# Optimization experiments

Hardware: AMD Instinct MI355X
Metric: run time of the kernel (lower is better)

Reference implementation:

```python
import jax, jax.numpy as jnp
import numpy as np

N = 50000      # nodes
E = 800000     # edges (before self-loops)
IN = 128       # in_channels
HID = 64       # hidden_channels
HEADS = 2
OUT = 128      # out_channels
NEG_SLOPE = 0.2


def setup_inputs() -> dict:
    key = jax.random.key(0)
    ks = jax.random.split(key, 12)
    p = lambda k, shape: jax.random.normal(k, shape, dtype=jnp.float32) * 0.05
    return {
        "x": jax.random.normal(ks[0], (N, IN), dtype=jnp.float32),
        "edge_index": jax.random.randint(ks[1], (2, E), 0, N, dtype=jnp.int32),
        "W1": p(ks[2], (IN, HEADS * HID)),
        "a_src1": p(ks[3], (HEADS, HID)),
        "a_dst1": p(ks[4], (HEADS, HID)),
        "b1": jnp.zeros((HEADS * HID,), dtype=jnp.float32),
        "W2": p(ks[5], (HEADS * HID, OUT)),
        "a_src2": p(ks[6], (1, OUT)),
        "a_dst2": p(ks[7], (1, OUT)),
        "b2": jnp.zeros((OUT,), dtype=jnp.float32),
    }


def _gat_conv(x, src, dst, W, a_src, a_dst, b, heads, out_c, concat):
    n = x.shape[0]
    h = (x @ W).reshape(n, heads, out_c)                # [N,H,C]
    al_s = jnp.sum(h * a_src, axis=-1)                  # [N,H]
    al_d = jnp.sum(h * a_dst, axis=-1)                  # [N,H]
    e = jax.nn.leaky_relu(al_s[src] + al_d[dst], NEG_SLOPE)  # [E',H]
    # softmax over edges grouped by destination node (numerically stable)
    e_max = jax.ops.segment_max(e, dst, num_segments=n)
    ee = jnp.exp(e - e_max[dst])
    denom = jax.ops.segment_sum(ee, dst, num_segments=n)
    alpha = ee / (denom[dst] + 1e-16)                   # [E',H]
    out = jax.ops.segment_sum(alpha[:, :, None] * h[src], dst, num_segments=n)  # [N,H,C]
    out = out.reshape(n, heads * out_c) if concat else out.mean(axis=1)
    return out + b


def reference(x, edge_index, W1, a_src1, a_dst1, b1, W2, a_src2, a_dst2, b2):
    n = x.shape[0]
    loops = jnp.arange(n, dtype=edge_index.dtype)       # PyG GATConv adds self-loops
    src = jnp.concatenate([edge_index[0], loops])
    dst = jnp.concatenate([edge_index[1], loops])
    h = jax.nn.elu(_gat_conv(x, src, dst, W1, a_src1, a_dst1, b1, HEADS, HID, True))
    return _gat_conv(h, src, dst, W2, a_src2, a_dst2, b2, 1, OUT, False)
```

## Files before the change

### kernel.cpp

```cpp
#include <hip/hip_runtime.h>
#include <hip/hip_bf16.h>
#include <math.h>

#define N_NODES 50000
#define NPAD 50048
#define N_EDGES 800000
#define NEG_SLOPE 0.2f
#define NBUCK ((N_NODES + 255) / 256)
#define CCHUNK 4096
#define DCAP 8192

__device__ inline float lrelu(float x) { return fmaxf(x, NEG_SLOPE * x); }

__device__ inline unsigned bf16rne(float f) {
    unsigned u = __float_as_uint(f);
    return (u + 0x7fffu + ((u >> 16) & 1u)) >> 16;
}
__device__ inline float bf2f(unsigned h) { return __uint_as_float(h << 16); }

__global__ void zerobuf_kernel(int* __restrict__ p) {
    int i = threadIdx.x;
    if (i < NBUCK) p[i] = 0;
}

__global__ __launch_bounds__(256) void bucketcount_kernel(const int* __restrict__ ei,
                                                          int* __restrict__ gbcnt) {
    __shared__ int lc[NBUCK];
    for (int i = threadIdx.x; i < NBUCK; i += 256) lc[i] = 0;
    __syncthreads();
    int stride = gridDim.x * 256;
    for (int e = blockIdx.x * 256 + threadIdx.x; e < N_EDGES; e += stride)
        atomicAdd(&lc[ei[N_EDGES + e] >> 8], 1);
    __syncthreads();
    for (int i = threadIdx.x; i < NBUCK; i += 256)
        if (lc[i]) atomicAdd(&gbcnt[i], lc[i]);
}

__global__ __launch_bounds__(256) void scan_convw_kernel(const int* __restrict__ gbcnt,
                                                         int* __restrict__ bbase,
                                                         int* __restrict__ bcur,
                                                         const float* __restrict__ W1,
                                                         unsigned short* __restrict__ w1h,
                                                         unsigned short* __restrict__ w1l,
                                                         const float* __restrict__ W2,
                                                         unsigned short* __restrict__ w2h,
                                                         unsigned short* __restrict__ w2l) {
    int b = blockIdx.x;
    int t = threadIdx.x;
    if (b == 0) {
        __shared__ int ss[256];
        int v = (t < NBUCK) ? gbcnt[t] : 0;
        ss[t] = v;
        __syncthreads();
        for (int d = 1; d < 256; d <<= 1) {
            int u = (t >= d) ? ss[t - d] : 0;
            __syncthreads();
            ss[t] += u;
            __syncthreads();
        }
        int excl = ss[t] - v;
        if (t < NBUCK) { bbase[t] = excl; bcur[t] = excl; }
        if (t == 0) bbase[NBUCK] = N_EDGES;
    } else {
        int idx = (b - 1) * 256 + t;
        const float* W = W1;
        unsigned short* th = w1h;
        unsigned short* tl = w1l;
        if (idx >= 128 * 128) { W = W2; th = w2h; tl = w2l; idx -= 128 * 128; }
        int c = idx >> 7, k = idx & 127;
        float v = W[(size_t)k * 128 + c];
        unsigned h = bf16rne(v);
        th[idx] = (unsigned short)h;
        tl[idx] = (unsigned short)bf16rne(v - bf2f(h));
    }
}

__global__ __launch_bounds__(256) void bucketscatter_kernel(const int* __restrict__ ei,
                                                            int* __restrict__ bcur,
                                                            unsigned* __restrict__ bpairs) {
    __shared__ int cnt[NBUCK], startl[NBUCK], baseg[NBUCK], cur2[NBUCK];
    __shared__ int ss[256];
    __shared__ unsigned stage[CCHUNK];
    int t = threadIdx.x;
    int e0 = blockIdx.x * CCHUNK;
    int nume = min(CCHUNK, N_EDGES - e0);
    for (int i = t; i < NBUCK; i += 256) { cnt[i] = 0; cur2[i] = 0; }
    __syncthreads();
    int src[CCHUNK / 256], dst[CCHUNK / 256];
    #pragma unroll
    for (int j = 0; j < CCHUNK / 256; ++j) {
        int idx = t + j * 256;
        if (idx < nume) {
            src[j] = ei[e0 + idx];
            dst[j] = ei[N_EDGES + e0 + idx];
            atomicAdd(&cnt[dst[j] >> 8], 1);
        } else dst[j] = -1;
    }
    __syncthreads();
    {
        int v = (t < NBUCK) ? cnt[t] : 0;
        ss[t] = v;
        __syncthreads();
        for (int d = 1; d < 256; d <<= 1) {
            int u = (t >= d) ? ss[t - d] : 0;
            __syncthreads();
            ss[t] += u;
            __syncthreads();
        }
        if (t < NBUCK) startl[t] = ss[t] - v;
    }
    __syncthreads();
    if (t < NBUCK && cnt[t] > 0) baseg[t] = atomicAdd(&bcur[t], cnt[t]);
    __syncthreads();
    #pragma unroll
    for (int j = 0; j < CCHUNK / 256; ++j) {
        if (dst[j] >= 0) {
            int b = dst[j] >> 8;
            int slot = startl[b] + atomicAdd(&cur2[b], 1);
            stage[slot] = (unsigned)src[j] | ((unsigned)dst[j] << 16);
        }
    }
    __syncthreads();
    for (int i = t; i < nume; i += 256) {
        unsigned pk = stage[i];
        int b = pk >> 24;
        bpairs[baseg[b] + (i - startl[b])] = pk;
    }
}

__global__ __launch_bounds__(256) void csrfinalize_kernel(const unsigned* __restrict__ bpairs,
                                                          const int* __restrict__ bbase,
                                                          int* __restrict__ ptr,
                                                          unsigned short* __restrict__ csr) {
    __shared__ int cnt[256], excl[256], cur[256];
    __shared__ int ss[256];
    __shared__ unsigned P[DCAP];
    int b = blockIdx.x, t = threadIdx.x;
    int bb = bbase[b], be = bbase[b + 1];
    int n = be - bb;
    int d0 = b << 8;
    int dmax = min(256, N_NODES - d0);
    bool fits = (n <= DCAP);
    cnt[t] = 0; cur[t] = 0;
    __syncthreads();
    for (int i = t; i < n; i += 256) {
        unsigned pk = bpairs[bb + i];
        if (fits) P[i] = pk;
        atomicAdd(&cnt[(pk >> 16) & 255], 1);
    }
    __syncthreads();
    {
        int v = cnt[t];
        ss[t] = v;
        __syncthreads();
        for (int d = 1; d < 256; d <<= 1) {
            int u = (t >= d) ? ss[t - d] : 0;
            __syncthreads();
            ss[t] += u;
            __syncthreads();
        }
        excl[t] = ss[t] - v;
    }
    __syncthreads();
    if (t < dmax) ptr[d0 + t] = bb + excl[t];
    if (b == NBUCK - 1 && t == 0) ptr[N_NODES] = N_EDGES;
    for (int i = t; i < n; i += 256) {
        unsigned pk = fits ? P[i] : bpairs[bb + i];
        int ld = (pk >> 16) & 255;
        int pos = bb + excl[ld] + atomicAdd(&cur[ld], 1);
        csr[pos] = (unsigned short)(pk & 0xFFFFu);
    }
}

template <int H, int AF32>
__global__ __launch_bounds__(256) void gemm_mfma_kernel(const unsigned short* __restrict__ Ah,
                                                        const unsigned short* __restrict__ Al,
                                                        const float* __restrict__ Af,
                                                        const unsigned short* __restrict__ Bh,
                                                        const unsigned short* __restrict__ Bl,
                                                        const float* __restrict__ asrc,
                                                        const float* __restrict__ adst,
                                                        unsigned short* __restrict__ Hb,
                                                        float* __restrict__ als,
                                                        float* __restrict__ ald,
                                                        int nrows) {
    using bf16x8 = __attribute__((ext_vector_type(8))) short;
    using f32x4  = __attribute__((ext_vector_type(4))) float;
    const int lane = threadIdx.x & 63;
    const int wv = threadIdx.x >> 6;
    const int l15 = lane & 15;
    const int g = lane >> 4;
    const int lk = g * 8;
    const int rowbase = blockIdx.x * 128 + wv * 32;
    const int r0c = min(rowbase + l15, nrows - 1);
    const int r1c = min(rowbase + 16 + l15, nrows - 1);

    f32x4 acc[2][8];
    #pragma unroll
    for (int rt = 0; rt < 2; ++rt)
        #pragma unroll
        for (int ct = 0; ct < 8; ++ct) acc[rt][ct] = (f32x4){0.f, 0.f, 0.f, 0.f};

    #pragma unroll
    for (int kc = 0; kc < 4; ++kc) {
        const int ko = kc * 32 + lk;
        bf16x8 ah0, ah1, al0, al1;
        if constexpr (AF32) {
            const float* b0 = Af + (size_t)r0c * 128 + ko;
            const float* b1 = Af + (size_t)r1c * 128 + ko;
            float4 u0 = *(const float4*)b0, u1 = *(const float4*)(b0 + 4);
            float4 v0 = *(const float4*)b1, v1 = *(const float4*)(b1 + 4);
            float a0[8] = {u0.x, u0.y, u0.z, u0.w, u1.x, u1.y, u1.z, u1.w};
            float a1[8] = {v0.x, v0.y, v0.z, v0.w, v1.x, v1.y, v1.z, v1.w};
            #pragma unroll
            for (int i = 0; i < 8; ++i) {
                unsigned h0 = bf16rne(a0[i]);
                ah0[i] = (short)h0; al0[i] = (short)bf16rne(a0[i] - bf2f(h0));
                unsigned h1 = bf16rne(a1[i]);
                ah1[i] = (short)h1; al1[i] = (short)bf16rne(a1[i] - bf2f(h1));
            }
        } else {
            ah0 = *(const bf16x8*)(Ah + (size_t)(rowbase + l15) * 128 + ko);
            ah1 = *(const bf16x8*)(Ah + (size_t)(rowbase + 16 + l15) * 128 + ko);
            al0 = *(const bf16x8*)(Al + (size_t)(rowbase + l15) * 128 + ko);
            al1 = *(const bf16x8*)(Al + (size_t)(rowbase + 16 + l15) * 128 + ko);
        }
        #pragma unroll
        for (int ct = 0; ct < 8; ++ct) {
            bf16x8 bh = *(const bf16x8*)(Bh + (size_t)(ct * 16 + l15) * 128 + ko);
            bf16x8 bl = *(const bf16x8*)(Bl + (size_t)(ct * 16 + l15) * 128 + ko);
            acc[0][ct] = __builtin_amdgcn_mfma_f32_16x16x32_bf16(ah0, bh, acc[0][ct], 0, 0, 0);
            acc[0][ct] = __builtin_amdgcn_mfma_f32_16x16x32_bf16(ah0, bl, acc[0][ct], 0, 0, 0);
            acc[0][ct] = __builtin_amdgcn_mfma_f32_16x16x32_bf16(al0, bh, acc[0][ct], 0, 0, 0);
            acc[1][ct] = __builtin_amdgcn_mfma_f32_16x16x32_bf16(ah1, bh, acc[1][ct], 0, 0, 0);
            acc[1][ct] = __builtin_amdgcn_mfma_f32_16x16x32_bf16(ah1, bl, acc[1][ct], 0, 0, 0);
            acc[1][ct] = __builtin_amdgcn_mfma_f32_16x16x32_bf16(al1, bh, acc[1][ct], 0, 0, 0);
        }
    }

    float as8[8], ad8[8];
    #pragma unroll
    for (int ct = 0; ct < 8; ++ct) { as8[ct] = asrc[ct * 16 + l15]; ad8[ct] = adst[ct * 16 + l15]; }

    #pragma unroll
    for (int rt = 0; rt < 2; ++rt) {
        #pragma unroll
        for (int ct = 0; ct < 8; ++ct) {
            #pragma unroll
            for (int j = 0; j < 4; ++j) {
                int row = rowbase + rt * 16 + g * 4 + j;
                if (row < nrows)
                    Hb[(size_t)row * 128 + ct * 16 + l15] = (unsigned short)bf16rne(acc[rt][ct][j]);
            }
        }
        #pragma unroll
        for (int j = 0; j < 4; ++j) {
            int row = rowbase + rt * 16 + g * 4 + j;
            if (H == 2) {
                float sp0 = 0.f, sp1 = 0.f, dp0 = 0.f, dp1 = 0.f;
                #pragma unroll
                for (int ct = 0; ct < 4; ++ct) { sp0 += acc[rt][ct][j] * as8[ct]; dp0 += acc[rt][ct][j] * ad8[ct]; }
                #pragma unroll
                for (int ct = 4; ct < 8; ++ct) { sp1 += acc[rt][ct][j] * as8[ct]; dp1 += acc[rt][ct][j] * ad8[ct]; }
                #pragma unroll
                for (int off = 1; off < 16; off <<= 1) {
                    sp0 += __shfl_xor(sp0, off); sp1 += __shfl_xor(sp1, off);
                    dp0 += __shfl_xor(dp0, off); dp1 += __shfl_xor(dp1, off);
                }
                if (l15 == 0 && row < nrows) {
                    als[(size_t)row * 2]     = sp0; als[(size_t)row * 2 + 1] = sp1;
                    ald[(size_t)row * 2]     = dp0; ald[(size_t)row * 2 + 1] = dp1;
                }
            } else {
                float sp = 0.f, dp = 0.f;
                #pragma unroll
                for (int ct = 0; ct < 8; ++ct) { sp += acc[rt][ct][j] * as8[ct]; dp += acc[rt][ct][j] * ad8[ct]; }
                #pragma unroll
                for (int off = 1; off < 16; off <<= 1) {
                    sp += __shfl_xor(sp, off); dp += __shfl_xor(dp, off);
                }
                if (l15 == 0 && row < nrows) { als[row] = sp; ald[row] = dp; }
            }
        }
    }
}

template <int H, int DO_ELU, int BSPLIT>
__global__ __launch_bounds__(256) void aggregate_kernel(const unsigned short* __restrict__ Hb,
                                                        const float* __restrict__ als,
                                                        const float* __restrict__ aldv,
                                                        const int* __restrict__ ptr,
                                                        const unsigned short* __restrict__ csr,
                                                        const float* __restrict__ bias,
                                                        float* __restrict__ out,
                                                        unsigned short* __restrict__ oh,
                                                        unsigned short* __restrict__ ol) {
    __shared__ int   s_src[4][64];
    __shared__ float s_p[4][H][64];
    const unsigned* __restrict__ Hb32 = (const unsigned*)Hb;
    const float2*   __restrict__ als2 = (const float2*)als;
    const int w = threadIdx.x >> 6;
    const int lane = threadIdx.x & 63;
    const int d = blockIdx.x * 4 + w;
    if (d >= N_NODES) return;
    const int head = (H == 2) ? (lane >> 5) : 0;

    int beg = ptr[d], end = ptr[d + 1];

    float ald0, ald1 = 0.f, es0, es1 = 0.f;
    if (H == 2) {
        float2 ta = *(const float2*)(aldv + (size_t)d * 2);
        float2 ts = als2[(unsigned)d];
        ald0 = ta.x; ald1 = ta.y;
        es0 = lrelu(ts.x + ald0); es1 = lrelu(ts.y + ald1);
    } else {
        ald0 = aldv[d]; es0 = lrelu(als[d] + ald0);
    }

    int k0 = beg + lane;
    int src0 = 0;
    float e0 = -INFINITY, e1 = -INFINITY;
    if (k0 < end) {
        src0 = csr[k0];
        if (H == 2) {
            float2 t = als2[(unsigned)src0];
            e0 = lrelu(t.x + ald0); e1 = lrelu(t.y + ald1);
        } else e0 = lrelu(als[(unsigned)src0] + ald0);
    }
    float m0 = fmaxf(es0, e0);
    float m1 = (H == 2) ? fmaxf(es1, e1) : 0.f;
    for (int k = k0 + 64; k < end; k += 64) {
        int s = csr[k];
        if (H == 2) {
            float2 t = als2[(unsigned)s];
            m0 = fmaxf(m0, lrelu(t.x + ald0));
            m1 = fmaxf(m1, lrelu(t.y + ald1));
        } else m0 = fmaxf(m0, lrelu(als[(unsigned)s] + ald0));
    }
    #pragma unroll
    for (int off = 32; off; off >>= 1) {
        m0 = fmaxf(m0, __shfl_xor(m0, off));
        if (H == 2) m1 = fmaxf(m1, __shfl_xor(m1, off));
    }

    float l0 = 0.f, l1 = 0.f;
    float ax0 = 0.f, ay0 = 0.f, ax1 = 0.f, ay1 = 0.f;
    float ax2 = 0.f, ay2 = 0.f, ax3 = 0.f, ay3 = 0.f;

    for (int t0 = beg; t0 < end; t0 += 64) {
        int cnt = min(64, end - t0);
        int k = t0 + lane;
        if (k < end) {
            int s; float f0, f1 = 0.f;
            if (t0 == beg) { s = src0; f0 = e0; f1 = e1; }
            else {
                s = csr[k];
                if (H == 2) {
                    float2 t = als2[(unsigned)s];
                    f0 = lrelu(t.x + ald0); f1 = lrelu(t.y + ald1);
                } else f0 = lrelu(als[(unsigned)s] + ald0);
            }
            float p0 = __expf(f0 - m0);
            l0 += p0;
            s_src[w][lane] = s;
            s_p[w][0][lane] = p0;
            if (H == 2) {
                float p1 = __expf(f1 - m1);
                l1 += p1;
                s_p[w][1][lane] = p1;
            }
        }
        int j = 0;
        for (; j + 3 < cnt; j += 4) {
            int sA = s_src[w][j],     sB = s_src[w][j + 1];
            int sC = s_src[w][j + 2], sD = s_src[w][j + 3];
            float pA = s_p[w][head][j],     pB = s_p[w][head][j + 1];
            float pC = s_p[w][head][j + 2], pD = s_p[w][head][j + 3];
            unsigned uA = Hb32[((unsigned)sA << 6) + lane];
            unsigned uB = Hb32[((unsigned)sB << 6) + lane];
            unsigned uC = Hb32[((unsigned)sC << 6) + lane];
            unsigned uD = Hb32[((unsigned)sD << 6) + lane];
            ax0 = fmaf(pA, __uint_as_float(uA << 16), ax0);
            ay0 = fmaf(pA, __uint_as_float(uA & 0xffff0000u), ay0);
            ax1 = fmaf(pB, __uint_as_float(uB << 16), ax1);
            ay1 = fmaf(pB, __uint_as_float(uB & 0xffff0000u), ay1);
            ax2 = fmaf(pC, __uint_as_float(uC << 16), ax2);
            ay2 = fmaf(pC, __uint_as_float(uC & 0xffff0000u), ay2);
            ax3 = fmaf(pD, __uint_as_float(uD << 16), ax3);
            ay3 = fmaf(pD, __uint_as_float(uD & 0xffff0000u), ay3);
        }
        for (; j < cnt; ++j) {
            int sA = s_src[w][j];
            float pA = s_p[w][head][j];
            unsigned uA = Hb32[((unsigned)sA << 6) + lane];
            ax0 = fmaf(pA, __uint_as_float(uA << 16), ax0);
            ay0 = fmaf(pA, __uint_as_float(uA & 0xffff0000u), ay0);
        }
    }

    float ax = (ax0 + ax1) + (ax2 + ax3);
    float ay = (ay0 + ay1) + (ay2 + ay3);
    float mh  = (head == 0) ? m0 : m1;
    float esh = (head == 0) ? es0 : es1;
    float psh = __expf(esh - mh);
    {
        unsigned u = Hb32[((unsigned)d << 6) + lane];
        ax = fmaf(psh, __uint_as_float(u << 16), ax);
        ay = fmaf(psh, __uint_as_float(u & 0xffff0000u), ay);
    }
    #pragma unroll
    for (int off = 32; off; off >>= 1) {
        l0 += __shfl_xor(l0, off);
        if (H == 2) l1 += __shfl_xor(l1, off);
    }
    float denom = ((head == 0) ? l0 : l1) + psh;
    float inv = 1.f / (denom + 1e-16f);
    float o0 = ax * inv + bias[2 * lane];
    float o1 = ay * inv + bias[2 * lane + 1];
    if (DO_ELU) {
        o0 = o0 > 0.f ? o0 : __expf(o0) - 1.f;
        o1 = o1 > 0.f ? o1 : __expf(o1) - 1.f;
    }
    if (BSPLIT) {
        unsigned h0 = bf16rne(o0), h1 = bf16rne(o1);
        ushort2 sh; sh.x = h0; sh.y = h1;
        ushort2 sl; sl.x = bf16rne(o0 - bf2f(h0)); sl.y = bf16rne(o1 - bf2f(h1));
        *(ushort2*)(oh + (size_t)d * 128 + 2 * lane) = sh;
        *(ushort2*)(ol + (size_t)d * 128 + 2 * lane) = sl;
    } else {
        ((float2*)(out + (size_t)d * 128))[lane] = make_float2(o0, o1);
    }
}

extern "C" void kernel_launch(void* const* d_in, const int* in_sizes, int n_in,
                              void* d_out, int out_size, void* d_ws, size_t ws_size,
                              hipStream_t stream) {
    const float* x      = (const float*)d_in[0];
    const int*   ei     = (const int*)d_in[1];
    const float* W1     = (const float*)d_in[2];
    const float* a_src1 = (const float*)d_in[3];
    const float* a_dst1 = (const float*)d_in[4];
    const float* b1     = (const float*)d_in[5];
    const float* W2     = (const float*)d_in[6];
    const float* a_src2 = (const float*)d_in[7];
    const float* a_dst2 = (const float*)d_in[8];
    const float* b2     = (const float*)d_in[9];
    float* out = (float*)d_out;

    char* ws = (char*)d_ws;
    size_t off = 0;
    auto alloc = [&](size_t bytes) { void* p = ws + off; off += (bytes + 255) & ~(size_t)255; return p; };
    int*      ptr    = (int*)alloc((N_NODES + 1) * sizeof(int));
    int*      gbcnt  = (int*)alloc(NBUCK * sizeof(int));
    int*      bbase  = (int*)alloc((NBUCK + 1) * sizeof(int));
    int*      bcur   = (int*)alloc(NBUCK * sizeof(int));
    unsigned* bpairs = (unsigned*)alloc((size_t)N_EDGES * sizeof(unsigned));
    unsigned short* csr = (unsigned short*)alloc((size_t)N_EDGES * sizeof(unsigned short));
    unsigned short* x2h = (unsigned short*)alloc((size_t)NPAD * 128 * 2);
    unsigned short* x2l = (unsigned short*)alloc((size_t)NPAD * 128 * 2);
    unsigned short* hb  = (unsigned short*)alloc((size_t)N_NODES * 128 * 2);
    unsigned short* w1h = (unsigned short*)alloc(128 * 128 * 2);
    unsigned short* w1l = (unsigned short*)alloc(128 * 128 * 2);
    unsigned short* w2h = (unsigned short*)alloc(128 * 128 * 2);
    unsigned short* w2l = (unsigned short*)alloc(128 * 128 * 2);
    float* als    = (float*)alloc(N_NODES * 2 * sizeof(float));
    float* ald    = (float*)alloc(N_NODES * 2 * sizeof(float));

    zerobuf_kernel<<<1, 256, 0, stream>>>(gbcnt);
    bucketcount_kernel<<<256, 256, 0, stream>>>(ei, gbcnt);
    scan_convw_kernel<<<129, 256, 0, stream>>>(gbcnt, bbase, bcur, W1, w1h, w1l, W2, w2h, w2l);
    bucketscatter_kernel<<<(N_EDGES + CCHUNK - 1) / CCHUNK, 256, 0, stream>>>(ei, bcur, bpairs);
    csrfinalize_kernel<<<NBUCK, 256, 0, stream>>>(bpairs, bbase, ptr, csr);

    int gblocks = NPAD / 128;
    int wblocks = (N_NODES + 3) / 4;

    gemm_mfma_kernel<2, 1><<<gblocks, 256, 0, stream>>>(nullptr, nullptr, x, w1h, w1l,
                                                        a_src1, a_dst1, hb, als, ald, N_NODES);
    aggregate_kernel<2, 1, 1><<<wblocks, 256, 0, stream>>>(hb, als, ald, ptr, csr, b1,
                                                           nullptr, x2h, x2l);

    gemm_mfma_kernel<1, 0><<<gblocks, 256, 0, stream>>>(x2h, x2l, nullptr, w2h, w2l,
                                                        a_src2, a_dst2, hb, als, ald, N_NODES);
    aggregate_kernel<1, 0, 0><<<wblocks, 256, 0, stream>>>(hb, als, ald, ptr, csr, b2,
                                                           out, nullptr, nullptr);
}
```

Before: 170.8 us.

## Process two destination nodes per wavefront with 8-byte feature gathers

Measured after the change: 170.2 us. About the same (-0.3%).

```diff
diff --git a/kernel.cpp b/kernel.cpp
--- a/kernel.cpp
+++ b/kernel.cpp
@@ -295,30 +295,34 @@
                                                         float* __restrict__ out,
                                                         unsigned short* __restrict__ oh,
                                                         unsigned short* __restrict__ ol) {
-    __shared__ int   s_src[4][64];
-    __shared__ float s_p[4][H][64];
-    const unsigned* __restrict__ Hb32 = (const unsigned*)Hb;
-    const float2*   __restrict__ als2 = (const float2*)als;
+    __shared__ int   s_src[4][2][34];
+    __shared__ float s_p[4][2][H][34];
+    const uint2*  __restrict__ Hb2  = (const uint2*)Hb;
+    const float2* __restrict__ als2 = (const float2*)als;
     const int w = threadIdx.x >> 6;
     const int lane = threadIdx.x & 63;
-    const int d = blockIdx.x * 4 + w;
-    if (d >= N_NODES) return;
-    const int head = (H == 2) ? (lane >> 5) : 0;
-
-    int beg = ptr[d], end = ptr[d + 1];
+    const int half = lane >> 5;
+    const int l31 = lane & 31;
+    const int headc = (H == 2) ? (l31 >> 4) : 0;
+
+    int d = blockIdx.x * 8 + w * 2 + half;
+    bool valid = d < N_NODES;
+    int dv = valid ? d : N_NODES - 1;
+    int beg = ptr[dv];
+    int end = valid ? ptr[dv + 1] : beg;
 
     float ald0, ald1 = 0.f, es0, es1 = 0.f;
     if (H == 2) {
-        float2 ta = *(const float2*)(aldv + (size_t)d * 2);
-        float2 ts = als2[(unsigned)d];
+        float2 ta = ((const float2*)aldv)[(unsigned)dv];
+        float2 ts = als2[(unsigned)dv];
         ald0 = ta.x; ald1 = ta.y;
         es0 = lrelu(ts.x + ald0); es1 = lrelu(ts.y + ald1);
     } else {
-        ald0 = aldv[d]; es0 = lrelu(als[d] + ald0);
-    }
-
-    int k0 = beg + lane;
-    int src0 = 0;
+        ald0 = aldv[dv]; es0 = lrelu(als[dv] + ald0);
+    }
+
+    int k0 = beg + l31;
+    int src0 = dv;
     float e0 = -INFINITY, e1 = -INFINITY;
     if (k0 < end) {
         src0 = csr[k0];
@@ -329,7 +333,7 @@
     }
     float m0 = fmaxf(es0, e0);
     float m1 = (H == 2) ? fmaxf(es1, e1) : 0.f;
-    for (int k = k0 + 64; k < end; k += 64) {
+    for (int k = k0 + 32; k < end; k += 32) {
         int s = csr[k];
         if (H == 2) {
             float2 t = als2[(unsigned)s];
@@ -338,97 +342,126 @@
         } else m0 = fmaxf(m0, lrelu(als[(unsigned)s] + ald0));
     }
     #pragma unroll
-    for (int off = 32; off; off >>= 1) {
+    for (int off = 16; off; off >>= 1) {
         m0 = fmaxf(m0, __shfl_xor(m0, off));
         if (H == 2) m1 = fmaxf(m1, __shfl_xor(m1, off));
     }
 
     float l0 = 0.f, l1 = 0.f;
-    float ax0 = 0.f, ay0 = 0.f, ax1 = 0.f, ay1 = 0.f;
-    float ax2 = 0.f, ay2 = 0.f, ax3 = 0.f, ay3 = 0.f;
-
-    for (int t0 = beg; t0 < end; t0 += 64) {
-        int cnt = min(64, end - t0);
-        int k = t0 + lane;
-        if (k < end) {
-            int s; float f0, f1 = 0.f;
-            if (t0 == beg) { s = src0; f0 = e0; f1 = e1; }
-            else {
-                s = csr[k];
-                if (H == 2) {
-                    float2 t = als2[(unsigned)s];
-                    f0 = lrelu(t.x + ald0); f1 = lrelu(t.y + ald1);
-                } else f0 = lrelu(als[(unsigned)s] + ald0);
+    float ac0[4], ac1[4], ac2[4], ac3[4];
+    #pragma unroll
+    for (int i = 0; i < 4; ++i) { ac0[i] = 0.f; ac1[i] = 0.f; ac2[i] = 0.f; ac3[i] = 0.f; }
+
+    for (int tt = 0; ; ++tt) {
+        int t0 = beg + tt * 32;
+        int degT = end - t0;
+        degT = degT < 0 ? 0 : (degT > 32 ? 32 : degT);
+        int jm = max(degT, __shfl_xor(degT, 32));
+        if (jm == 0) break;
+        {
+            int k = t0 + l31;
+            int s = dv;
+            float p0v = 0.f, p1v = 0.f;
+            if (k < end) {
+                float f0, f1 = 0.f;
+                if (tt == 0) { s = src0; f0 = e0; f1 = e1; }
+                else {
+                    s = csr[k];
+                    if (H == 2) {
+                        float2 t = als2[(unsigned)s];
+                        f0 = lrelu(t.x + ald0); f1 = lrelu(t.y + ald1);
+                    } else f0 = lrelu(als[(unsigned)s] + ald0);
+                }
+                p0v = __expf(f0 - m0);
+                l0 += p0v;
+                if (H == 2) { p1v = __expf(f1 - m1); l1 += p1v; }
             }
-            float p0 = __expf(f0 - m0);
-            l0 += p0;
-            s_src[w][lane] = s;
-            s_p[w][0][lane] = p0;
-            if (H == 2) {
-                float p1 = __expf(f1 - m1);
-                l1 += p1;
-                s_p[w][1][lane] = p1;
-            }
+            s_src[w][half][l31] = s;
+            s_p[w][half][0][l31] = p0v;
+            if (H == 2) s_p[w][half][1][l31] = p1v;
         }
         int j = 0;
-        for (; j + 3 < cnt; j += 4) {
-            int sA = s_src[w][j],     sB = s_src[w][j + 1];
-            int sC = s_src[w][j + 2], sD = s_src[w][j + 3];
-            float pA = s_p[w][head][j],     pB = s_p[w][head][j + 1];
-            float pC = s_p[w][head][j + 2], pD = s_p[w][head][j + 3];
-            unsigned uA = Hb32[((unsigned)sA << 6) + lane];
-            unsigned uB = Hb32[((unsigned)sB << 6) + lane];
-            unsigned uC = Hb32[((unsigned)sC << 6) + lane];
-            unsigned uD = Hb32[((unsigned)sD << 6) + lane];
-            ax0 = fmaf(pA, __uint_as_float(uA << 16), ax0);
-            ay0 = fmaf(pA, __uint_as_float(uA & 0xffff0000u), ay0);
-            ax1 = fmaf(pB, __uint_as_float(uB << 16), ax1);
-            ay1 = fmaf(pB, __uint_as_float(uB & 0xffff0000u), ay1);
-            ax2 = fmaf(pC, __uint_as_float(uC << 16), ax2);
-            ay2 = fmaf(pC, __uint_as_float(uC & 0xffff0000u), ay2);
-            ax3 = fmaf(pD, __uint_as_float(uD << 16), ax3);
-            ay3 = fmaf(pD, __uint_as_float(uD & 0xffff0000u), ay3);
-        }
-        for (; j < cnt; ++j) {
-            int sA = s_src[w][j];
-            float pA = s_p[w][head][j];
-            unsigned uA = Hb32[((unsigned)sA << 6) + lane];
-            ax0 = fmaf(pA, __uint_as_float(uA << 16), ax0);
-            ay0 = fmaf(pA, __uint_as_float(uA & 0xffff0000u), ay0);
-        }
-    }
-
-    float ax = (ax0 + ax1) + (ax2 + ax3);
-    float ay = (ay0 + ay1) + (ay2 + ay3);
-    float mh  = (head == 0) ? m0 : m1;
-    float esh = (head == 0) ? es0 : es1;
+        for (; j + 3 < jm; j += 4) {
+            int sA = s_src[w][half][j],     sB = s_src[w][half][j + 1];
+            int sC = s_src[w][half][j + 2], sD = s_src[w][half][j + 3];
+            float pA = s_p[w][half][headc][j],     pB = s_p[w][half][headc][j + 1];
+            float pC = s_p[w][half][headc][j + 2], pD = s_p[w][half][headc][j + 3];
+            uint2 uA = Hb2[((unsigned)sA << 5) + l31];
+            uint2 uB = Hb2[((unsigned)sB << 5) + l31];
+            uint2 uC = Hb2[((unsigned)sC << 5) + l31];
+            uint2 uD = Hb2[((unsigned)sD << 5) + l31];
+            ac0[0] = fmaf(pA, __uint_as_float(uA.x << 16), ac0[0]);
+            ac0[1] = fmaf(pA, __uint_as_float(uA.x & 0xffff0000u), ac0[1]);
+            ac0[2] = fmaf(pA, __uint_as_float(uA.y << 16), ac0[2]);
+            ac0[3] = fmaf(pA, __uint_as_float(uA.y & 0xffff0000u), ac0[3]);
+            ac1[0] = fmaf(pB, __uint_as_float(uB.x << 16), ac1[0]);
+            ac1[1] = fmaf(pB, __uint_as_float(uB.x & 0xffff0000u), ac1[1]);
+            ac1[2] = fmaf(pB, __uint_as_float(uB.y << 16), ac1[2]);
+            ac1[3] = fmaf(pB, __uint_as_float(uB.y & 0xffff0000u), ac1[3]);
+            ac2[0] = fmaf(pC, __uint_as_float(uC.x << 16), ac2[0]);
+            ac2[1] = fmaf(pC, __uint_as_float(uC.x & 0xffff0000u), ac2[1]);
+            ac2[2] = fmaf(pC, __uint_as_float(uC.y << 16), ac2[2]);
+            ac2[3] = fmaf(pC, __uint_as_float(uC.y & 0xffff0000u), ac2[3]);
+            ac3[0] = fmaf(pD, __uint_as_float(uD.x << 16), ac3[0]);
+            ac3[1] = fmaf(pD, __uint_as_float(uD.x & 0xffff0000u), ac3[1]);
+            ac3[2] = fmaf(pD, __uint_as_float(uD.y << 16), ac3[2]);
+            ac3[3] = fmaf(pD, __uint_as_float(uD.y & 0xffff0000u), ac3[3]);
+        }
+        for (; j < jm; ++j) {
+            int sA = s_src[w][half][j];
+            float pA = s_p[w][half][headc][j];
+            uint2 uA = Hb2[((unsigned)sA << 5) + l31];
+            ac0[0] = fmaf(pA, __uint_as_float(uA.x << 16), ac0[0]);
+            ac0[1] = fmaf(pA, __uint_as_float(uA.x & 0xffff0000u), ac0[1]);
+            ac0[2] = fmaf(pA, __uint_as_float(uA.y << 16), ac0[2]);
+            ac0[3] = fmaf(pA, __uint_as_float(uA.y & 0xffff0000u), ac0[3]);
+        }
+    }
+
+    float acc[4];
+    #pragma unroll
+    for (int i = 0; i < 4; ++i) acc[i] = (ac0[i] + ac1[i]) + (ac2[i] + ac3[i]);
+
+    float mh  = (headc == 0) ? m0 : m1;
+    float esh = (headc == 0) ? es0 : es1;
     float psh = __expf(esh - mh);
     {
-        unsigned u = Hb32[((unsigned)d << 6) + lane];
-        ax = fmaf(psh, __uint_as_float(u << 16), ax);
-        ay = fmaf(psh, __uint_as_float(u & 0xffff0000u), ay);
-    }
-    #pragma unroll
-    for (int off = 32; off; off >>= 1) {
+        uint2 u = Hb2[((unsigned)dv << 5) + l31];
+        acc[0] = fmaf(psh, __uint_as_float(u.x << 16), acc[0]);
+        acc[1] = fmaf(psh, __uint_as_float(u.x & 0xffff0000u), acc[1]);
+        acc[2] = fmaf(psh, __uint_as_float(u.y << 16), acc[2]);
+        acc[3] = fmaf(psh, __uint_as_float(u.y & 0xffff0000u), acc[3]);
+    }
+    #pragma unroll
+    for (int off = 16; off; off >>= 1) {
         l0 += __shfl_xor(l0, off);
         if (H == 2) l1 += __shfl_xor(l1, off);
     }
-    float denom = ((head == 0) ? l0 : l1) + psh;
+    float denom = ((headc == 0) ? l0 : l1) + psh;
     float inv = 1.f / (denom + 1e-16f);
-    float o0 = ax * inv + bias[2 * lane];
-    float o1 = ay * inv + bias[2 * lane + 1];
+    float4 b4 = *(const float4*)(bias + 4 * l31);
+    float o0 = acc[0] * inv + b4.x;
+    float o1 = acc[1] * inv + b4.y;
+    float o2 = acc[2] * inv + b4.z;
+    float o3 = acc[3] * inv + b4.w;
     if (DO_ELU) {
         o0 = o0 > 0.f ? o0 : __expf(o0) - 1.f;
         o1 = o1 > 0.f ? o1 : __expf(o1) - 1.f;
-    }
-    if (BSPLIT) {
-        unsigned h0 = bf16rne(o0), h1 = bf16rne(o1);
-        ushort2 sh; sh.x = h0; sh.y = h1;
-        ushort2 sl; sl.x = bf16rne(o0 - bf2f(h0)); sl.y = bf16rne(o1 - bf2f(h1));
-        *(ushort2*)(oh + (size_t)d * 128 + 2 * lane) = sh;
-        *(ushort2*)(ol + (size_t)d * 128 + 2 * lane) = sl;
-    } else {
-        ((float2*)(out + (size_t)d * 128))[lane] = make_float2(o0, o1);
+        o2 = o2 > 0.f ? o2 : __expf(o2) - 1.f;
+        o3 = o3 > 0.f ? o3 : __expf(o3) - 1.f;
+    }
+    if (valid) {
+        if (BSPLIT) {
+            unsigned h0 = bf16rne(o0), h1 = bf16rne(o1), h2 = bf16rne(o2), h3 = bf16rne(o3);
+            ushort4 sh; sh.x = h0; sh.y = h1; sh.z = h2; sh.w = h3;
+            ushort4 sl;
+            sl.x = bf16rne(o0 - bf2f(h0)); sl.y = bf16rne(o1 - bf2f(h1));
+            sl.z = bf16rne(o2 - bf2f(h2)); sl.w = bf16rne(o3 - bf2f(h3));
+            *(ushort4*)(oh + (size_t)dv * 128 + 4 * l31) = sh;
+            *(ushort4*)(ol + (size_t)dv * 128 + 4 * l31) = sl;
+        } else {
+            *(float4*)(out + (size_t)dv * 128 + 4 * l31) = make_float4(o0, o1, o2, o3);
+        }
     }
 }
 
@@ -473,7 +506,7 @@
     csrfinalize_kernel<<<NBUCK, 256, 0, stream>>>(bpairs, bbase, ptr, csr);
 
     int gblocks = NPAD / 128;
-    int wblocks = (N_NODES + 3) / 4;
+    int wblocks = (N_NODES + 7) / 8;
 
     gemm_mfma_kernel<2, 1><<<gblocks, 256, 0, stream>>>(nullptr, nullptr, x, w1h, w1l,
                                                         a_src1, a_dst1, hb, als, ald, N_NODES);
```
